# Optimization experiments

Hardware: AMD Instinct MI355X
Metric: run time of the kernel (lower is better)

The kernel has to match this reference:

```python
import jax, jax.numpy as jnp
import numpy as np

N = 50000      # nodes
E = 800000     # edges (avg degree 16)
IN = 128       # in_channels
OUT = 64       # out_channels
K = 2          # propagation hops


def setup_inputs() -> dict:
    key = jax.random.key(0)
    k1, k2, k3 = jax.random.split(key, 3)
    x = jax.random.normal(k1, (N, IN), dtype=jnp.float32)
    edge_index = jax.random.randint(k2, (2, E), 0, N, dtype=jnp.int32)
    # SGConv's internal Linear(in, out): weight [OUT, IN], bias [OUT]
    W = jax.random.normal(k3, (OUT, IN), dtype=jnp.float32) / np.sqrt(IN)
    b = jnp.zeros((OUT,), dtype=jnp.float32)
    return {"x": x, "edge_index": edge_index, "W": W, "b": b}


def reference(x, edge_index, W, b):
    # GCN normalization with self-loops (PyG gcn_norm, add_self_loops=True)
    row, col = edge_index[0], edge_index[1]
    loops = jnp.arange(N, dtype=edge_index.dtype)
    row = jnp.concatenate([row, loops])   # source nodes
    col = jnp.concatenate([col, loops])   # target nodes
    ones = jnp.ones((E + N,), dtype=x.dtype)
    deg = jax.ops.segment_sum(ones, col, num_segments=N)          # in-degree incl. self-loop
    deg_inv_sqrt = jnp.where(deg > 0, jax.lax.rsqrt(deg), 0.0)
    norm = deg_inv_sqrt[row] * deg_inv_sqrt[col]                  # [E+N]

    # K-hop propagation: x <- D^{-1/2} (A+I) D^{-1/2} x
    for _ in range(K):
        x = jax.ops.segment_sum(x[row] * norm[:, None], col, num_segments=N)

    # final linear; dropout is identity in eval mode (training=False)
    return x @ W.T + b
```

## Files before the change

### kernel.cpp

```cpp
#include <hip/hip_runtime.h>
#include <hip/hip_bf16.h>
#include <hip/hip_fp16.h>

#define IN_CH 128
#define OUT_CH 64
#define NB 256
#define CHUNK_CAP 3200
#define SORT_CAP 6144

typedef _Float16 hh2 __attribute__((ext_vector_type(2)));

__global__ void __launch_bounds__(256) fat1_kernel(const float* __restrict__ x,
                                                   const float* __restrict__ W,
                                                   __half* __restrict__ z0,
                                                   const int* __restrict__ col,
                                                   int* __restrict__ rawcnt,
                                                   int n, int E, int chunk, int GB) {
    __shared__ char smraw[64 * 66 * 2 * 2 * 2];
    int t = threadIdx.x;

    if (blockIdx.x >= GB) {
        int* h = (int*)smraw;
        int blk = blockIdx.x - GB;
        h[t] = 0;
        __syncthreads();
        int s = blk * chunk, e = min(s + chunk, E);
        for (int i = s + t; i < e; i += 256)
            atomicAdd(&h[col[i] >> 8], 1);
        __syncthreads();
        rawcnt[blk * 256 + t] = h[t];
        return;
    }

    hh2* Xs = (hh2*)smraw;
    hh2* Ws = Xs + 64 * 66;
    int m0 = blockIdx.x * 64;
#pragma unroll
    for (int r = 0; r < 8; ++r) {
        int f = t + 256 * r;
        int o = f >> 5, kq = f & 31;
        float4 w = ((const float4*)W)[f];
        Ws[o * 66 + kq * 2]     = hh2{(_Float16)w.x, (_Float16)w.y};
        Ws[o * 66 + kq * 2 + 1] = hh2{(_Float16)w.z, (_Float16)w.w};
    }
#pragma unroll
    for (int r = 0; r < 8; ++r) {
        int f = t + 256 * r;
        int node = f >> 5, kq = f & 31;
        int gv = min(m0 + node, n - 1);
        float4 xv = ((const float4*)(x + (size_t)gv * IN_CH))[kq];
        Xs[node * 66 + kq * 2]     = hh2{(_Float16)xv.x, (_Float16)xv.y};
        Xs[node * 66 + kq * 2 + 1] = hh2{(_Float16)xv.z, (_Float16)xv.w};
    }
    __syncthreads();
    int tx = t & 15, ty = t >> 4;
    float acc[4][4];
#pragma unroll
    for (int i = 0; i < 4; ++i)
#pragma unroll
        for (int j = 0; j < 4; ++j) acc[i][j] = 0.f;
#pragma unroll 4
    for (int kq = 0; kq < 32; ++kq) {
        hh2 xa0[4], xa1[4], wb0[4], wb1[4];
#pragma unroll
        for (int i = 0; i < 4; ++i) {
            int base = (tx + 16 * i) * 66 + kq * 2;
            xa0[i] = Xs[base]; xa1[i] = Xs[base + 1];
        }
#pragma unroll
        for (int j = 0; j < 4; ++j) {
            int base = (ty * 4 + j) * 66 + kq * 2;
            wb0[j] = Ws[base]; wb1[j] = Ws[base + 1];
        }
#pragma unroll
        for (int i = 0; i < 4; ++i)
#pragma unroll
            for (int j = 0; j < 4; ++j) {
                float s = acc[i][j];
                s = __builtin_amdgcn_fdot2(xa0[i], wb0[j], s, false);
                s = __builtin_amdgcn_fdot2(xa1[i], wb1[j], s, false);
                acc[i][j] = s;
            }
    }
#pragma unroll
    for (int i = 0; i < 4; ++i) {
        int v = m0 + tx + 16 * i;
        if (v < n) {
            union { __half2 h[2]; float2 f; } u;
            u.h[0] = __floats2half2_rn(acc[i][0], acc[i][1]);
            u.h[1] = __floats2half2_rn(acc[i][2], acc[i][3]);
            *(float2*)&z0[(size_t)v * OUT_CH + ty * 4] = u.f;
        }
    }
}

__global__ void __launch_bounds__(512) scatter_kernel(const int* __restrict__ row,
                                                      const int* __restrict__ col,
                                                      const int* __restrict__ rawcnt,
                                                      unsigned int* __restrict__ tmp,
                                                      int E, int chunk) {
    __shared__ int psT[256];
    __shared__ int psC[256];
    __shared__ int biasl[256];
    __shared__ int curl[256];
    __shared__ unsigned int vall[CHUNK_CAP];
    __shared__ int destl[CHUNK_CAP];
    int blk = blockIdx.x, tid = threadIdx.x;
    int T = 0, P = 0, C = 0;
    if (tid < 256) {
        for (int b = 0; b < NB; ++b) {
            int v = rawcnt[b * 256 + tid];
            T += v;
            P += (b < blk) ? v : 0;
            C = (b == blk) ? v : C;
        }
        psT[tid] = T; psC[tid] = C;
    }
    __syncthreads();
    for (int d = 1; d < 256; d <<= 1) {
        int a = 0, c2 = 0;
        if (tid < 256 && tid >= d) { a = psT[tid - d]; c2 = psC[tid - d]; }
        __syncthreads();
        if (tid < 256 && tid >= d) { psT[tid] += a; psC[tid] += c2; }
        __syncthreads();
    }
    if (tid < 256) {
        int B = psT[tid] - T;
        int loff = psC[tid] - C;
        biasl[tid] = B + P - loff;
        curl[tid] = loff;
    }
    __syncthreads();
    int s = blk * chunk, e = min(s + chunk, E);
    int csize = e - s;
    if (csize <= CHUNK_CAP) {
        for (int i = s + tid; i < e; i += 512) {
            int c = col[i], r = row[i];
            int k = c >> 8;
            int p = atomicAdd(&curl[k], 1);
            vall[p]  = ((unsigned)(c & 255) << 16) | (unsigned)r;
            destl[p] = biasl[k] + p;
        }
        __syncthreads();
        for (int j = tid; j < csize; j += 512)
            tmp[destl[j]] = vall[j];
    } else {
        for (int i = s + tid; i < e; i += 512) {
            int c = col[i], r = row[i];
            int k = c >> 8;
            int p = atomicAdd(&curl[k], 1);
            tmp[biasl[k] + p] = ((unsigned)(c & 255) << 16) | (unsigned)r;
        }
    }
}

__global__ void __launch_bounds__(512) sort_kernel(const unsigned int* __restrict__ tmp,
                                                   const int* __restrict__ rawcnt,
                                                   int* __restrict__ off,
                                                   float* __restrict__ dis,
                                                   unsigned short* __restrict__ eidx,
                                                   int nbkt, int E, int n) {
    __shared__ int bs[256];
    __shared__ int cntT[256];
    __shared__ int cntl[256];
    __shared__ int sc[256];
    __shared__ int posr[256];
    __shared__ unsigned short el[SORT_CAP];
    int b = blockIdx.x, tid = threadIdx.x;
    int T = 0;
    if (tid < 256) {
        for (int bb = 0; bb < NB; ++bb)
            T += rawcnt[bb * 256 + tid];
        bs[tid] = T; cntT[tid] = T;
    }
    __syncthreads();
    for (int d = 1; d < 256; d <<= 1) {
        int a = 0;
        if (tid < 256 && tid >= d) a = bs[tid - d];
        __syncthreads();
        if (tid < 256 && tid >= d) bs[tid] += a;
        __syncthreads();
    }
    if (tid < 256) bs[tid] -= T;
    if (tid < 256) cntl[tid] = 0;
    __syncthreads();
    int s = bs[b];
    int cnt = cntT[b];
    int e = s + cnt;
    for (int i = s + tid; i < e; i += 512)
        atomicAdd(&cntl[tmp[i] >> 16], 1);
    __syncthreads();
    int c = 0;
    if (tid < 256) { c = cntl[tid]; sc[tid] = c; }
    __syncthreads();
    for (int d = 1; d < 256; d <<= 1) {
        int a = 0;
        if (tid < 256 && tid >= d) a = sc[tid - d];
        __syncthreads();
        if (tid < 256 && tid >= d) sc[tid] += a;
        __syncthreads();
    }
    if (tid < 256) {
        int excl = sc[tid] - c;
        int gid = (b << 8) + tid;
        if (gid < n) {
            off[gid] = s + excl;
            dis[gid] = rsqrtf((float)(c + 1));
        }
        posr[tid] = excl;
    }
    if (b == 0 && tid == 0) off[n] = E;
    __syncthreads();
    bool staged = (cnt <= SORT_CAP);
    if (staged) {
        for (int i = s + tid; i < e; i += 512) {
            unsigned int w = tmp[i];
            int p = atomicAdd(&posr[w >> 16], 1);
            el[p] = (unsigned short)(w & 0xFFFFu);
        }
        __syncthreads();
        for (int i = tid; i < cnt; i += 512)
            eidx[s + i] = el[i];
    } else {
        for (int i = s + tid; i < e; i += 512) {
            unsigned int w = tmp[i];
            int p = atomicAdd(&posr[w >> 16], 1);
            eidx[s + p] = (unsigned short)(w & 0xFFFFu);
        }
    }
}

#define ACC8(raw) { const __half2* h2_ = (const __half2*)&(raw);              \
    float2 f0_ = __half22float2(h2_[0]), f1_ = __half22float2(h2_[1]);        \
    float2 f2_ = __half22float2(h2_[2]), f3_ = __half22float2(h2_[3]);        \
    a0 += f0_.x; a1 += f0_.y; a2 += f1_.x; a3 += f1_.y;                       \
    a4 += f2_.x; a5 += f2_.y; a6 += f3_.x; a7 += f3_.y; }

#define FMA8(raw, dr) { const __half2* h2_ = (const __half2*)&(raw);          \
    float2 f0_ = __half22float2(h2_[0]), f1_ = __half22float2(h2_[1]);        \
    float2 f2_ = __half22float2(h2_[2]), f3_ = __half22float2(h2_[3]);        \
    a0 = fmaf(dr, f0_.x, a0); a1 = fmaf(dr, f0_.y, a1);                       \
    a2 = fmaf(dr, f1_.x, a2); a3 = fmaf(dr, f1_.y, a3);                       \
    a4 = fmaf(dr, f2_.x, a4); a5 = fmaf(dr, f2_.y, a5);                       \
    a6 = fmaf(dr, f3_.x, a6); a7 = fmaf(dr, f3_.y, a7); }

template <int MODE>
__global__ void __launch_bounds__(256) hop_kernel(const __half* __restrict__ zin,
                                                  void* __restrict__ out,
                                                  const unsigned short* __restrict__ eidx,
                                                  const int* __restrict__ off,
                                                  const float* __restrict__ dis,
                                                  const float* __restrict__ bias, int n) {
    int v = (int)((blockIdx.x * 256 + threadIdx.x) >> 6);
    if (v >= n) return;
    int lane = threadIdx.x & 63;
    int grp = lane >> 3;
    int sub = lane & 7;
    int s = off[v], e = off[v + 1];
    float dv = dis[v];
    float a0 = 0.f, a1 = 0.f, a2 = 0.f, a3 = 0.f;
    float a4 = 0.f, a5 = 0.f, a6 = 0.f, a7 = 0.f;
    if (grp == 0) {
        float4 raw = ((const float4*)(zin + (size_t)v * OUT_CH))[sub];
        if (MODE == 0) { FMA8(raw, dv); } else { ACC8(raw); }
    }
    int i0 = s + grp;
    int i1 = i0 + 8, i2 = i0 + 16, i3 = i0 + 24;
    bool h0 = i0 < e, h1 = i1 < e, h2 = i2 < e, h3 = i3 < e;
    int r0 = h0 ? (int)eidx[i0] : 0;
    int r1 = h1 ? (int)eidx[i1] : 0;
    int r2 = h2 ? (int)eidx[i2] : 0;
    int r3 = h3 ? (int)eidx[i3] : 0;
    float d0 = 1.f, d1 = 1.f, d2 = 1.f, d3 = 1.f;
    if (MODE == 0) {
        if (h0) d0 = dis[r0];
        if (h1) d1 = dis[r1];
        if (h2) d2 = dis[r2];
        if (h3) d3 = dis[r3];
    }
    float4 rA = make_float4(0.f, 0.f, 0.f, 0.f);
    float4 rB = make_float4(0.f, 0.f, 0.f, 0.f);
    float4 rC = make_float4(0.f, 0.f, 0.f, 0.f);
    float4 rD = make_float4(0.f, 0.f, 0.f, 0.f);
    if (h0) rA = ((const float4*)(zin + (size_t)r0 * OUT_CH))[sub];
    if (h1) rB = ((const float4*)(zin + (size_t)r1 * OUT_CH))[sub];
    if (h2) rC = ((const float4*)(zin + (size_t)r2 * OUT_CH))[sub];
    if (h3) rD = ((const float4*)(zin + (size_t)r3 * OUT_CH))[sub];
    if (MODE == 0) {
        FMA8(rA, d0); FMA8(rB, d1); FMA8(rC, d2); FMA8(rD, d3);
    } else {
        ACC8(rA); ACC8(rB); ACC8(rC); ACC8(rD);
    }
    if (e - s > 32) {
        int j0 = s + 32 + grp, j1 = j0 + 8;
        bool g0 = j0 < e, g1 = j1 < e;
        int q0 = g0 ? (int)eidx[j0] : 0;
        int q1 = g1 ? (int)eidx[j1] : 0;
        while (g0) {
            int k0 = j0 + 16, k1 = j1 + 16;
            bool f0 = k0 < e, f1 = k1 < e;
            int p0 = f0 ? (int)eidx[k0] : 0;
            int p1 = f1 ? (int)eidx[k1] : 0;
            float dq0 = 1.f, dq1 = 1.f;
            if (MODE == 0) {
                if (g0) dq0 = dis[q0];
                if (g1) dq1 = dis[q1];
            }
            float4 xA = make_float4(0.f, 0.f, 0.f, 0.f);
            float4 xB = make_float4(0.f, 0.f, 0.f, 0.f);
            if (g0) xA = ((const float4*)(zin + (size_t)q0 * OUT_CH))[sub];
            if (g1) xB = ((const float4*)(zin + (size_t)q1 * OUT_CH))[sub];
            if (MODE == 0) { FMA8(xA, dq0); FMA8(xB, dq1); }
            else           { ACC8(xA); ACC8(xB); }
            j0 = k0; j1 = k1; q0 = p0; q1 = p1; g0 = f0; g1 = f1;
        }
    }
#pragma unroll
    for (int m = 8; m <= 32; m <<= 1) {
        a0 += __shfl_xor(a0, m, 64); a1 += __shfl_xor(a1, m, 64);
        a2 += __shfl_xor(a2, m, 64); a3 += __shfl_xor(a3, m, 64);
        a4 += __shfl_xor(a4, m, 64); a5 += __shfl_xor(a5, m, 64);
        a6 += __shfl_xor(a6, m, 64); a7 += __shfl_xor(a7, m, 64);
    }
    if (grp == 0) {
        if (MODE == 0) {
            float sc = dv * dv;
            union { __half2 h[4]; float4 f; } u;
            u.h[0] = __floats2half2_rn(sc * a0, sc * a1);
            u.h[1] = __floats2half2_rn(sc * a2, sc * a3);
            u.h[2] = __floats2half2_rn(sc * a4, sc * a5);
            u.h[3] = __floats2half2_rn(sc * a6, sc * a7);
            ((float4*)((__half*)out + (size_t)v * OUT_CH))[sub] = u.f;
        } else {
            const float4* bp = (const float4*)(bias + sub * 8);
            float4 b0 = bp[0], b1 = bp[1];
            float* op = (float*)out + (size_t)v * OUT_CH + sub * 8;
            *(float4*)op = make_float4(fmaf(dv, a0, b0.x), fmaf(dv, a1, b0.y),
                                       fmaf(dv, a2, b0.z), fmaf(dv, a3, b0.w));
            *(float4*)(op + 4) = make_float4(fmaf(dv, a4, b1.x), fmaf(dv, a5, b1.y),
                                             fmaf(dv, a6, b1.z), fmaf(dv, a7, b1.w));
        }
    }
}

extern "C" void kernel_launch(void* const* d_in, const int* in_sizes, int n_in,
                              void* d_out, int out_size, void* d_ws, size_t ws_size,
                              hipStream_t stream) {
    const float* x = (const float*)d_in[0];
    const int* ei = (const int*)d_in[1];
    const float* W = (const float*)d_in[2];
    const float* b = (const float*)d_in[3];
    int n = in_sizes[0] / IN_CH;
    int E = in_sizes[1] / 2;
    const int* row = ei;
    const int* col = ei + E;

    char* ws = (char*)d_ws;
    size_t o = 0;
    auto alloc = [&](size_t bytes) -> void* {
        void* p = ws + o;
        o += (bytes + 255) & ~(size_t)255;
        return p;
    };
    int nbkt = (n + 255) >> 8;
    int chunk = (E + NB - 1) / NB;
    int GB = (n + 63) / 64;

    int*            rawcnt = (int*)alloc((size_t)NB * 256 * 4);
    unsigned int*   tmp    = (unsigned int*)alloc((size_t)E * 4);
    int*            off    = (int*)alloc((size_t)(n + 1) * 4);
    float*          dis    = (float*)alloc((size_t)n * 4);
    unsigned short* eidx   = (unsigned short*)alloc((size_t)E * 2);
    __half*         zA     = (__half*)alloc((size_t)n * OUT_CH * 2);
    __half*         zB     = (__half*)alloc((size_t)n * OUT_CH * 2);

    fat1_kernel<<<GB + NB, 256, 0, stream>>>(x, W, zA, col, rawcnt, n, E, chunk, GB);
    scatter_kernel<<<NB, 512, 0, stream>>>(row, col, rawcnt, tmp, E, chunk);
    sort_kernel<<<nbkt, 512, 0, stream>>>(tmp, rawcnt, off, dis, eidx, nbkt, E, n);
    int hopBlocks = (n + 3) / 4;
    hop_kernel<0><<<hopBlocks, 256, 0, stream>>>(zA, zB, eidx, off, dis, nullptr, n);
    hop_kernel<1><<<hopBlocks, 256, 0, stream>>>(zB, d_out, eidx, off, dis, b, n);
}
```

Baseline: 161.2 us.

## Prescale projected features by source degree in sort kernel, drop per-edge dis gathers

The GEMM now writes fp32 z0, and the sort kernel, which already computes each node's inverse-sqrt degree, writes fp16 zA pre-multiplied by that source scale. The first hop kernel then accumulates plain sums instead of gathering dis[src] per edge and doing FMAs. This removes a random gather per edge in hop 0. In exchange it adds an fp32 write and read of the full projected feature array.

After: 165.1 us. +2.4%, slower.

```diff
diff --git a/kernel.cpp b/kernel.cpp
--- a/kernel.cpp
+++ b/kernel.cpp
@@ -10,12 +10,12 @@
 
 typedef _Float16 hh2 __attribute__((ext_vector_type(2)));
 
-__global__ void __launch_bounds__(256) fat1_kernel(const float* __restrict__ x,
-                                                   const float* __restrict__ W,
-                                                   __half* __restrict__ z0,
-                                                   const int* __restrict__ col,
-                                                   int* __restrict__ rawcnt,
-                                                   int n, int E, int chunk, int GB) {
+__global__ void __launch_bounds__(256) fat_kernel(const float* __restrict__ x,
+                                                  const float* __restrict__ W,
+                                                  float* __restrict__ z0,
+                                                  const int* __restrict__ col,
+                                                  int* __restrict__ blkcnt,
+                                                  int n, int E, int chunk, int GB) {
     __shared__ char smraw[64 * 66 * 2 * 2 * 2];
     int t = threadIdx.x;
 
@@ -28,7 +28,7 @@
         for (int i = s + t; i < e; i += 256)
             atomicAdd(&h[col[i] >> 8], 1);
         __syncthreads();
-        rawcnt[blk * 256 + t] = h[t];
+        blkcnt[blk * 256 + t] = h[t];
         return;
     }
 
@@ -59,6 +59,7 @@
     for (int i = 0; i < 4; ++i)
 #pragma unroll
         for (int j = 0; j < 4; ++j) acc[i][j] = 0.f;
+
 #pragma unroll 4
     for (int kq = 0; kq < 32; ++kq) {
         hh2 xa0[4], xa1[4], wb0[4], wb1[4];
@@ -85,18 +86,15 @@
 #pragma unroll
     for (int i = 0; i < 4; ++i) {
         int v = m0 + tx + 16 * i;
-        if (v < n) {
-            union { __half2 h[2]; float2 f; } u;
-            u.h[0] = __floats2half2_rn(acc[i][0], acc[i][1]);
-            u.h[1] = __floats2half2_rn(acc[i][2], acc[i][3]);
-            *(float2*)&z0[(size_t)v * OUT_CH + ty * 4] = u.f;
-        }
+        if (v < n)
+            *(float4*)&z0[(size_t)v * OUT_CH + ty * 4] =
+                make_float4(acc[i][0], acc[i][1], acc[i][2], acc[i][3]);
     }
 }
 
 __global__ void __launch_bounds__(512) scatter_kernel(const int* __restrict__ row,
                                                       const int* __restrict__ col,
-                                                      const int* __restrict__ rawcnt,
+                                                      const int* __restrict__ blkcnt,
                                                       unsigned int* __restrict__ tmp,
                                                       int E, int chunk) {
     __shared__ int psT[256];
@@ -109,7 +107,7 @@
     int T = 0, P = 0, C = 0;
     if (tid < 256) {
         for (int b = 0; b < NB; ++b) {
-            int v = rawcnt[b * 256 + tid];
+            int v = blkcnt[b * 256 + tid];
             T += v;
             P += (b < blk) ? v : 0;
             C = (b == blk) ? v : C;
@@ -155,22 +153,25 @@
 }
 
 __global__ void __launch_bounds__(512) sort_kernel(const unsigned int* __restrict__ tmp,
-                                                   const int* __restrict__ rawcnt,
+                                                   const int* __restrict__ blkcnt,
+                                                   const float* __restrict__ z0,
                                                    int* __restrict__ off,
                                                    float* __restrict__ dis,
                                                    unsigned short* __restrict__ eidx,
-                                                   int nbkt, int E, int n) {
+                                                   __half* __restrict__ zA,
+                                                   int E, int n) {
     __shared__ int bs[256];
     __shared__ int cntT[256];
     __shared__ int cntl[256];
     __shared__ int sc[256];
     __shared__ int posr[256];
+    __shared__ float dl[256];
     __shared__ unsigned short el[SORT_CAP];
     int b = blockIdx.x, tid = threadIdx.x;
     int T = 0;
     if (tid < 256) {
         for (int bb = 0; bb < NB; ++bb)
-            T += rawcnt[bb * 256 + tid];
+            T += blkcnt[bb * 256 + tid];
         bs[tid] = T; cntT[tid] = T;
     }
     __syncthreads();
@@ -203,11 +204,13 @@
     if (tid < 256) {
         int excl = sc[tid] - c;
         int gid = (b << 8) + tid;
+        float dv = rsqrtf((float)(c + 1));
         if (gid < n) {
             off[gid] = s + excl;
-            dis[gid] = rsqrtf((float)(c + 1));
+            dis[gid] = dv;
         }
         posr[tid] = excl;
+        dl[tid] = dv;
     }
     if (b == 0 && tid == 0) off[n] = E;
     __syncthreads();
@@ -228,6 +231,19 @@
             eidx[s + p] = (unsigned short)(w & 0xFFFFu);
         }
     }
+    const float4* z04 = (const float4*)z0;
+    for (int f = tid; f < 256 * 16; f += 512) {
+        int r = f >> 4, cc = f & 15;
+        int v = (b << 8) + r;
+        if (v < n) {
+            float4 zz = z04[(size_t)v * 16 + cc];
+            float sv = dl[r];
+            union { __half2 h[2]; float2 fo; } u;
+            u.h[0] = __floats2half2_rn(sv * zz.x, sv * zz.y);
+            u.h[1] = __floats2half2_rn(sv * zz.z, sv * zz.w);
+            *(float2*)&zA[(size_t)v * OUT_CH + cc * 4] = u.fo;
+        }
+    }
 }
 
 #define ACC8(raw) { const __half2* h2_ = (const __half2*)&(raw);              \
@@ -235,14 +251,6 @@
     float2 f2_ = __half22float2(h2_[2]), f3_ = __half22float2(h2_[3]);        \
     a0 += f0_.x; a1 += f0_.y; a2 += f1_.x; a3 += f1_.y;                       \
     a4 += f2_.x; a5 += f2_.y; a6 += f3_.x; a7 += f3_.y; }
-
-#define FMA8(raw, dr) { const __half2* h2_ = (const __half2*)&(raw);          \
-    float2 f0_ = __half22float2(h2_[0]), f1_ = __half22float2(h2_[1]);        \
-    float2 f2_ = __half22float2(h2_[2]), f3_ = __half22float2(h2_[3]);        \
-    a0 = fmaf(dr, f0_.x, a0); a1 = fmaf(dr, f0_.y, a1);                       \
-    a2 = fmaf(dr, f1_.x, a2); a3 = fmaf(dr, f1_.y, a3);                       \
-    a4 = fmaf(dr, f2_.x, a4); a5 = fmaf(dr, f2_.y, a5);                       \
-    a6 = fmaf(dr, f3_.x, a6); a7 = fmaf(dr, f3_.y, a7); }
 
 template <int MODE>
 __global__ void __launch_bounds__(256) hop_kernel(const __half* __restrict__ zin,
@@ -262,7 +270,7 @@
     float a4 = 0.f, a5 = 0.f, a6 = 0.f, a7 = 0.f;
     if (grp == 0) {
         float4 raw = ((const float4*)(zin + (size_t)v * OUT_CH))[sub];
-        if (MODE == 0) { FMA8(raw, dv); } else { ACC8(raw); }
+        ACC8(raw);
     }
     int i0 = s + grp;
     int i1 = i0 + 8, i2 = i0 + 16, i3 = i0 + 24;
@@ -271,13 +279,6 @@
     int r1 = h1 ? (int)eidx[i1] : 0;
     int r2 = h2 ? (int)eidx[i2] : 0;
     int r3 = h3 ? (int)eidx[i3] : 0;
-    float d0 = 1.f, d1 = 1.f, d2 = 1.f, d3 = 1.f;
-    if (MODE == 0) {
-        if (h0) d0 = dis[r0];
-        if (h1) d1 = dis[r1];
-        if (h2) d2 = dis[r2];
-        if (h3) d3 = dis[r3];
-    }
     float4 rA = make_float4(0.f, 0.f, 0.f, 0.f);
     float4 rB = make_float4(0.f, 0.f, 0.f, 0.f);
     float4 rC = make_float4(0.f, 0.f, 0.f, 0.f);
@@ -286,11 +287,7 @@
     if (h1) rB = ((const float4*)(zin + (size_t)r1 * OUT_CH))[sub];
     if (h2) rC = ((const float4*)(zin + (size_t)r2 * OUT_CH))[sub];
     if (h3) rD = ((const float4*)(zin + (size_t)r3 * OUT_CH))[sub];
-    if (MODE == 0) {
-        FMA8(rA, d0); FMA8(rB, d1); FMA8(rC, d2); FMA8(rD, d3);
-    } else {
-        ACC8(rA); ACC8(rB); ACC8(rC); ACC8(rD);
-    }
+    ACC8(rA); ACC8(rB); ACC8(rC); ACC8(rD);
     if (e - s > 32) {
         int j0 = s + 32 + grp, j1 = j0 + 8;
         bool g0 = j0 < e, g1 = j1 < e;
@@ -301,17 +298,11 @@
             bool f0 = k0 < e, f1 = k1 < e;
             int p0 = f0 ? (int)eidx[k0] : 0;
             int p1 = f1 ? (int)eidx[k1] : 0;
-            float dq0 = 1.f, dq1 = 1.f;
-            if (MODE == 0) {
-                if (g0) dq0 = dis[q0];
-                if (g1) dq1 = dis[q1];
-            }
             float4 xA = make_float4(0.f, 0.f, 0.f, 0.f);
             float4 xB = make_float4(0.f, 0.f, 0.f, 0.f);
             if (g0) xA = ((const float4*)(zin + (size_t)q0 * OUT_CH))[sub];
             if (g1) xB = ((const float4*)(zin + (size_t)q1 * OUT_CH))[sub];
-            if (MODE == 0) { FMA8(xA, dq0); FMA8(xB, dq1); }
-            else           { ACC8(xA); ACC8(xB); }
+            ACC8(xA); ACC8(xB);
             j0 = k0; j1 = k1; q0 = p0; q1 = p1; g0 = f0; g1 = f1;
         }
     }
@@ -366,17 +357,18 @@
     int chunk = (E + NB - 1) / NB;
     int GB = (n + 63) / 64;
 
-    int*            rawcnt = (int*)alloc((size_t)NB * 256 * 4);
+    int*            blkcnt = (int*)alloc((size_t)NB * 256 * 4);
     unsigned int*   tmp    = (unsigned int*)alloc((size_t)E * 4);
     int*            off    = (int*)alloc((size_t)(n + 1) * 4);
     float*          dis    = (float*)alloc((size_t)n * 4);
     unsigned short* eidx   = (unsigned short*)alloc((size_t)E * 2);
+    float*          z0     = (float*)alloc((size_t)n * OUT_CH * 4);
     __half*         zA     = (__half*)alloc((size_t)n * OUT_CH * 2);
     __half*         zB     = (__half*)alloc((size_t)n * OUT_CH * 2);
 
-    fat1_kernel<<<GB + NB, 256, 0, stream>>>(x, W, zA, col, rawcnt, n, E, chunk, GB);
-    scatter_kernel<<<NB, 512, 0, stream>>>(row, col, rawcnt, tmp, E, chunk);
-    sort_kernel<<<nbkt, 512, 0, stream>>>(tmp, rawcnt, off, dis, eidx, nbkt, E, n);
+    fat_kernel<<<GB + NB, 256, 0, stream>>>(x, W, z0, col, blkcnt, n, E, chunk, GB);
+    scatter_kernel<<<NB, 512, 0, stream>>>(row, col, blkcnt, tmp, E, chunk);
+    sort_kernel<<<nbkt, 512, 0, stream>>>(tmp, blkcnt, z0, off, dis, eidx, zA, E, n);
     int hopBlocks = (n + 3) / 4;
     hop_kernel<0><<<hopBlocks, 256, 0, stream>>>(zA, zB, eidx, off, dis, nullptr, n);
     hop_kernel<1><<<hopBlocks, 256, 0, stream>>>(zB, d_out, eidx, off, dis, b, n);
```
